# Kernel tuning notes

Measured on AMD Instinct MI355X. Metric: run time of the kernel, lower is better.

## Reference

```python
import jax, jax.numpy as jnp
import numpy as np

N = 50000      # nodes
DEG = 16       # avg degree
E = N * DEG    # edges
FIN = 128
FQK = 64
FV = 64
H = 8


def setup_inputs() -> dict:
    key = jax.random.key(0)
    k1, k2, k3, k4 = jax.random.split(key, 4)
    x = jax.random.normal(k1, (N, FIN), dtype=jnp.float32)
    # torch Linear(Fin, 2*Fqk+Fv, bias=False); stored here as [Fin, Ftot] so y = x @ W
    W = jax.random.normal(k2, (FIN, 2 * FQK + FV), dtype=jnp.float32) / np.sqrt(FIN)
    # edges: src sorted and covering all nodes (required by scatter_softmax semantics)
    src = jnp.repeat(jnp.arange(N, dtype=jnp.int32), DEG)
    dest = jax.random.randint(k3, (E,), 0, N, dtype=jnp.int32)
    ei = jnp.stack([src, dest])  # [2, E]
    batch = jnp.sort(jax.random.randint(k4, (N,), 0, 64, dtype=jnp.int32))
    return {"x": x, "W": W, "batch": batch, "ei": ei}


def reference(x, W, batch, ei):
    n = x.shape[0]
    Fh = FQK // H   # per-head qk dim
    Fhv = FV // H   # per-head v dim
    scaling = float(Fh) ** (-0.5)

    qkv = x @ W  # [N, 2*Fqk+Fv]
    q, k, v = jnp.split(qkv, [FQK, 2 * FQK], axis=-1)
    q = (q * scaling).reshape(n, H, Fh)
    k = k.reshape(n, H, Fh)
    v = v.reshape(n, H, Fhv)

    src, dest = ei[0], ei[1]
    qs = q[src]   # [E, H, Fh]
    ks = k[dest]  # [E, H, Fh]
    vs = v[dest]  # [E, H, Fhv]

    aw = jnp.einsum("ehf,ehf->eh", qs, ks)  # per-edge per-head logits

    # segment softmax over src (numerically stable, same math as exp/segsum(exp))
    amax = jax.ops.segment_max(aw, src, num_segments=n)
    ex = jnp.exp(aw - amax[src])
    denom = jax.ops.segment_sum(ex, src, num_segments=n)
    aw = ex / denom[src]  # [E, H]

    out = jax.ops.segment_sum(aw[:, :, None] * vs, src, num_segments=n)  # [N, H, Fhv]
    return out.reshape(n, H * Fhv)
```

## Files before the change

### kernel.cpp

```cpp
#include <hip/hip_runtime.h>
#include <math.h>

#define N_NODES 50000
#define DEG 16
#define E_EDGES (N_NODES * DEG)
#define FIN 128
#define FTOT 192
#define FQK 64
#define FV 64
#define H 8

typedef __attribute__((ext_vector_type(8))) short short8;
typedef __attribute__((ext_vector_type(4))) float float4v;

__device__ inline unsigned short f2bf(float f) {
    unsigned int u = __float_as_uint(f);
    unsigned int r = u + 0x7fffu + ((u >> 16) & 1u);
    return (unsigned short)(r >> 16);
}
__device__ inline float bf2f(unsigned short b) {
    return __uint_as_float(((unsigned int)b) << 16);
}

#define LDB 136
#define LDC 194

__global__ __launch_bounds__(256) void gemm_qkv(const float* __restrict__ x,
                                                const float* __restrict__ W,
                                                unsigned short* __restrict__ qkv) {
    __shared__ unsigned short Bt[FTOT * LDB];
    unsigned short* Ct = Bt;
    const int tid = threadIdx.x;

#pragma unroll
    for (int i = 0; i < 12; i++) {
        int idx = tid + i * 256;
        int n = idx % 192, kg = idx / 192;
        int k0 = kg * 8;
        unsigned short tmp[8];
#pragma unroll
        for (int j = 0; j < 8; j++)
            tmp[j] = f2bf(W[(k0 + j) * FTOT + n]);
        *(uint4*)(&Bt[n * LDB + k0]) = *(const uint4*)tmp;
    }

    const int wave = tid >> 6, lane = tid & 63;
    const int m = lane & 15, q = lane >> 4;
    const int row = blockIdx.x * 64 + wave * 16 + m;
    const int rowc = min(row, N_NODES - 1);

    short8 a[4];
    const float* xr = x + rowc * FIN;
#pragma unroll
    for (int s = 0; s < 4; s++) {
        float4v f0 = *(const float4v*)(xr + s * 32 + q * 8);
        float4v f1 = *(const float4v*)(xr + s * 32 + q * 8 + 4);
        short8 av;
        av[0] = (short)f2bf(f0.x); av[1] = (short)f2bf(f0.y);
        av[2] = (short)f2bf(f0.z); av[3] = (short)f2bf(f0.w);
        av[4] = (short)f2bf(f1.x); av[5] = (short)f2bf(f1.y);
        av[6] = (short)f2bf(f1.z); av[7] = (short)f2bf(f1.w);
        a[s] = av;
    }
    __syncthreads();

    float4v acc[12];
#pragma unroll
    for (int ct = 0; ct < 12; ct++) acc[ct] = (float4v){0.f, 0.f, 0.f, 0.f};
#pragma unroll
    for (int ct = 0; ct < 12; ct++) {
#pragma unroll
        for (int s = 0; s < 4; s++) {
            short8 b = *(const short8*)(&Bt[(ct * 16 + m) * LDB + s * 32 + q * 8]);
            acc[ct] = __builtin_amdgcn_mfma_f32_16x16x32_bf16(a[s], b, acc[ct], 0, 0, 0);
        }
    }
    __syncthreads();

    const int lrow0 = wave * 16 + q * 4;
#pragma unroll
    for (int ct = 0; ct < 12; ct++) {
        const int col = ct * 16 + m;
        int off; float scale;
        if (col < FQK)          { off = col;                      scale = 0.35355339059327373f; }
        else if (col < 2 * FQK) { off = 64 + 2 * (col - 64);      scale = 1.f; }
        else                    { off = 64 + 2 * (col - 128) + 1; scale = 1.f; }
#pragma unroll
        for (int i = 0; i < 4; i++)
            Ct[(lrow0 + i) * LDC + off] = f2bf(acc[ct][i] * scale);
    }
    __syncthreads();

    unsigned int* qg = (unsigned int*)qkv;
    const int base = blockIdx.x * 64;
#pragma unroll
    for (int i = 0; i < 24; i++) {
        int l = tid + i * 256;
        int r = l / 96, dw = l - r * 96;
        if (base + r < N_NODES)
            qg[(size_t)(base + r) * 96 + dw] = *(const unsigned int*)(&Ct[r * LDC + 2 * dw]);
    }
}

__global__ __launch_bounds__(256) void attn(const unsigned short* __restrict__ qkv,
                                            const int* __restrict__ dest,
                                            float* __restrict__ out) {
    const int node = blockIdx.x * 4 + (threadIdx.x >> 6);
    const int lane = threadIdx.x & 63;
    const int half = lane >> 5;
    const int l = lane & 31;
    if (node >= N_NODES) return;

    const unsigned int qw = *(const unsigned int*)(qkv + node * FTOT + 2 * l);
    const float q0 = __uint_as_float(qw << 16);
    const float q1 = __uint_as_float(qw & 0xffff0000u);
    const int dj = dest[node * DEG + (lane & 15)];

    uint2 kv[8];
#pragma unroll
    for (int t = 0; t < 8; t++) {
        const int d = __shfl(dj, 2 * t + half, 64);
        kv[t] = *(const uint2*)(qkv + d * FTOT + 64 + 4 * l);
    }

    float lg[8];
#pragma unroll
    for (int t = 0; t < 8; t++) {
        const float k0 = __uint_as_float(kv[t].x << 16);
        const float k1 = __uint_as_float(kv[t].y << 16);
        float p = fmaf(q0, k0, q1 * k1);
        p += __shfl_xor(p, 1, 64);
        p += __shfl_xor(p, 2, 64);
        lg[t] = p;
    }
    float mx = lg[0];
#pragma unroll
    for (int t = 1; t < 8; t++) mx = fmaxf(mx, lg[t]);
    float s = 0.f, o0 = 0.f, o1 = 0.f;
#pragma unroll
    for (int t = 0; t < 8; t++) {
        const float p = __expf(lg[t] - mx);
        s += p;
        o0 = fmaf(p, __uint_as_float(kv[t].x & 0xffff0000u), o0);
        o1 = fmaf(p, __uint_as_float(kv[t].y & 0xffff0000u), o1);
    }
    const float mo = __shfl_xor(mx, 32, 64);
    const float mn = fmaxf(mx, mo);
    const float f = __expf(mx - mn);
    s *= f; o0 *= f; o1 *= f;
    s  += __shfl_xor(s, 32, 64);
    o0 += __shfl_xor(o0, 32, 64);
    o1 += __shfl_xor(o1, 32, 64);
    if (half == 0) {
        float2 r; r.x = o0 / s; r.y = o1 / s;
        *(float2*)(out + node * 64 + 2 * l) = r;
    }
}

extern "C" void kernel_launch(void* const* d_in, const int* in_sizes, int n_in,
                              void* d_out, int out_size, void* d_ws, size_t ws_size,
                              hipStream_t stream) {
    const float* x = (const float*)d_in[0];
    const float* W = (const float*)d_in[1];
    const int* ei = (const int*)d_in[3];
    const int* dest = ei + E_EDGES;
    float* out = (float*)d_out;

    unsigned short* qkv = (unsigned short*)d_ws;

    gemm_qkv<<<(N_NODES + 63) / 64, 256, 0, stream>>>(x, W, qkv);
    attn<<<(N_NODES + 3) / 4, 256, 0, stream>>>(qkv, dest, out);
}
```

Baseline: 112.6 us.

## Store K and V as separate contiguous blocks and load V after softmax max

The GEMM epilogue now writes qkv in natural column order instead of interleaving K and V per element. The attention kernel then issues separate 4-byte K loads, and after reducing the max across both halves it issues 4-byte V loads, which removes the rescaling step. Each gathered neighbor now costs two dependent narrower loads instead of one 8-byte load, trading memory-level parallelism and transactions for simpler softmax math.

```diff
diff --git a/kernel.cpp b/kernel.cpp
--- a/kernel.cpp
+++ b/kernel.cpp
@@ -18,9 +18,8 @@
     unsigned int r = u + 0x7fffu + ((u >> 16) & 1u);
     return (unsigned short)(r >> 16);
 }
-__device__ inline float bf2f(unsigned short b) {
-    return __uint_as_float(((unsigned int)b) << 16);
-}
+__device__ inline float bflo(unsigned int w) { return __uint_as_float(w << 16); }
+__device__ inline float bfhi(unsigned int w) { return __uint_as_float(w & 0xffff0000u); }
 
 #define LDB 136
 #define LDC 194
@@ -81,13 +80,10 @@
 #pragma unroll
     for (int ct = 0; ct < 12; ct++) {
         const int col = ct * 16 + m;
-        int off; float scale;
-        if (col < FQK)          { off = col;                      scale = 0.35355339059327373f; }
-        else if (col < 2 * FQK) { off = 64 + 2 * (col - 64);      scale = 1.f; }
-        else                    { off = 64 + 2 * (col - 128) + 1; scale = 1.f; }
+        const float scale = (col < FQK) ? 0.35355339059327373f : 1.f;
 #pragma unroll
         for (int i = 0; i < 4; i++)
-            Ct[(lrow0 + i) * LDC + off] = f2bf(acc[ct][i] * scale);
+            Ct[(lrow0 + i) * LDC + col] = f2bf(acc[ct][i] * scale);
     }
     __syncthreads();
 
@@ -112,23 +108,22 @@
     if (node >= N_NODES) return;
 
     const unsigned int qw = *(const unsigned int*)(qkv + node * FTOT + 2 * l);
-    const float q0 = __uint_as_float(qw << 16);
-    const float q1 = __uint_as_float(qw & 0xffff0000u);
+    const float q0 = bflo(qw), q1 = bfhi(qw);
     const int dj = dest[node * DEG + (lane & 15)];
 
-    uint2 kv[8];
+    int doff[8];
+    unsigned int kk[8];
 #pragma unroll
     for (int t = 0; t < 8; t++) {
         const int d = __shfl(dj, 2 * t + half, 64);
-        kv[t] = *(const uint2*)(qkv + d * FTOT + 64 + 4 * l);
+        doff[t] = d * FTOT;
+        kk[t] = *(const unsigned int*)(qkv + doff[t] + 64 + 2 * l);
     }
 
     float lg[8];
 #pragma unroll
     for (int t = 0; t < 8; t++) {
-        const float k0 = __uint_as_float(kv[t].x << 16);
-        const float k1 = __uint_as_float(kv[t].y << 16);
-        float p = fmaf(q0, k0, q1 * k1);
+        float p = fmaf(q0, bflo(kk[t]), q1 * bfhi(kk[t]));
         p += __shfl_xor(p, 1, 64);
         p += __shfl_xor(p, 2, 64);
         lg[t] = p;
@@ -136,18 +131,21 @@
     float mx = lg[0];
 #pragma unroll
     for (int t = 1; t < 8; t++) mx = fmaxf(mx, lg[t]);
+    mx = fmaxf(mx, __shfl_xor(mx, 32, 64));
+
+    unsigned int vv[8];
+#pragma unroll
+    for (int t = 0; t < 8; t++)
+        vv[t] = *(const unsigned int*)(qkv + doff[t] + 128 + 2 * l);
+
     float s = 0.f, o0 = 0.f, o1 = 0.f;
 #pragma unroll
     for (int t = 0; t < 8; t++) {
         const float p = __expf(lg[t] - mx);
         s += p;
-        o0 = fmaf(p, __uint_as_float(kv[t].x & 0xffff0000u), o0);
-        o1 = fmaf(p, __uint_as_float(kv[t].y & 0xffff0000u), o1);
+        o0 = fmaf(p, bflo(vv[t]), o0);
+        o1 = fmaf(p, bfhi(vv[t]), o1);
     }
-    const float mo = __shfl_xor(mx, 32, 64);
-    const float mn = fmaxf(mx, mo);
-    const float f = __expf(mx - mn);
-    s *= f; o0 *= f; o1 *= f;
     s  += __shfl_xor(s, 32, 64);
     o0 += __shfl_xor(o0, 32, 64);
     o1 += __shfl_xor(o1, 32, 64);
```

After: 113.8 us. No clear change (+1.0%).
